# Kernel optimization log

Measured on AMD Instinct MI355X. Metric: run time of the kernel, lower is better.

The kernel has to match this reference:

```python
import jax, jax.numpy as jnp
import numpy as np

N_NODES = 150000
N_EDGES = 4800000
IN_DIM, HID_DIM, OUT_DIM = 1433, 16, 7


def setup_inputs() -> dict:
    key = jax.random.key(0)
    ks = jax.random.split(key, 8)
    features = jax.random.normal(ks[0], (N_NODES, IN_DIM), dtype=jnp.float32)
    edge_src = jax.random.randint(ks[1], (N_EDGES,), 0, N_NODES, dtype=jnp.int32)
    edge_dst = jax.random.randint(ks[2], (N_EDGES,), 0, N_NODES, dtype=jnp.int32)
    adj_vals = jax.random.uniform(ks[3], (N_EDGES,), dtype=jnp.float32)
    W1 = jax.random.normal(ks[4], (IN_DIM, HID_DIM), dtype=jnp.float32) * (1.0 / np.sqrt(IN_DIM))
    b1 = jnp.zeros((HID_DIM,), dtype=jnp.float32)
    W2 = jax.random.normal(ks[5], (HID_DIM, OUT_DIM), dtype=jnp.float32) * (1.0 / np.sqrt(HID_DIM))
    b2 = jnp.zeros((OUT_DIM,), dtype=jnp.float32)
    return {"features": features, "edge_src": edge_src, "edge_dst": edge_dst,
            "adj_vals": adj_vals, "W1": W1, "b1": b1, "W2": W2, "b2": b2}


def _gcn_layer(x, edge_src, edge_dst, adj_vals, W, b):
    # h = A_hat @ (x @ W) + b ; dense transform first since in_dim >= out_dim
    xw = x @ W                                   # [N, d_out]
    msg = adj_vals[:, None] * xw[edge_src]       # [E, d_out] gather
    agg = jax.ops.segment_sum(msg, edge_dst, num_segments=x.shape[0])  # scatter-add
    return agg + b


def reference(features, edge_src, edge_dst, adj_vals, W1, b1, W2, b2):
    h1 = jax.nn.relu(_gcn_layer(features, edge_src, edge_dst, adj_vals, W1, b1))
    # dropout in original forward is a no-op (result discarded) -> omitted
    h2 = _gcn_layer(h1, edge_src, edge_dst, adj_vals, W2, b2)
    return jax.nn.log_softmax(h2, axis=1)
```

## Files before the change

### kernel.cpp

```cpp
#include <hip/hip_runtime.h>
#include <float.h>
#include <stdint.h>

#define IN_DIM 1433
#define HID 16
#define OUTD 7

#define KC 32
#define GROWS 128
#define NT ((IN_DIM + KC - 1) / KC)
#define KLAST (IN_DIM - (NT - 1) * KC)

__global__ __launch_bounds__(256, 4) void gemm1_kernel(
    const float* __restrict__ feat, const float* __restrict__ W1,
    float* __restrict__ xw1, int N)
{
    __shared__ float xs[2][GROWS * KC];
    const int t = threadIdx.x;
    const int lane = t & 63;
    const int wid = t >> 6;
    const int row0 = blockIdx.x * GROWS;
    const long maxElem = (long)N * IN_DIM - 1;

    const int r  = t & (GROWS - 1);
    const int jh = t >> 7;
    const int rx = r & 31;

    float acc[8];
#pragma unroll
    for (int j = 0; j < 8; ++j) acc[j] = 0.f;

    const int jhu = __builtin_amdgcn_readfirstlane(jh);
    const float* __restrict__ wptr = W1 + jhu * 8;

    const int l5 = lane >> 5;
    const int c  = lane & 31;

    auto stage = [&](int buf, int k0) {
#pragma unroll
        for (int i = 0; i < 16; ++i) {
            const int rr = wid * 32 + i * 2 + l5;
            long elem = (long)(row0 + rr) * IN_DIM + k0 + (c ^ (rr & 31));
            if (elem > maxElem) elem = maxElem;
            const float* gp = feat + elem;
            float* lp = &xs[buf][(wid * 32 + i * 2) * KC];
            __builtin_amdgcn_global_load_lds(
                (const __attribute__((address_space(1))) void*)gp,
                (__attribute__((address_space(3))) void*)lp, 4, 0, 0);
        }
    };

#define COMPUTE(buf, k0v, KMAX)                                          \
    {                                                                    \
        const float* xrow = &xs[buf][r * KC];                            \
        const float* wk = wptr + (size_t)(k0v) * HID;                    \
        _Pragma("unroll")                                                \
        for (int kk = 0; kk < (KMAX); ++kk) {                            \
            const float x = xrow[kk ^ rx];                               \
            const float4 wa = *(const float4*)(wk + kk * HID);           \
            const float4 wb = *(const float4*)(wk + kk * HID + 4);       \
            acc[0] += x * wa.x; acc[1] += x * wa.y;                      \
            acc[2] += x * wa.z; acc[3] += x * wa.w;                      \
            acc[4] += x * wb.x; acc[5] += x * wb.y;                      \
            acc[6] += x * wb.z; acc[7] += x * wb.w;                      \
        }                                                                \
    }

    stage(0, 0);
    __syncthreads();
    for (int it = 0; it < NT - 1; ++it) {
        const int cur = it & 1;
        stage(cur ^ 1, (it + 1) * KC);
        COMPUTE(cur, it * KC, KC);
        __syncthreads();
    }
    COMPUTE((NT - 1) & 1, (NT - 1) * KC, KLAST);
#undef COMPUTE

    const int grow = row0 + r;
    if (grow < N) {
        float4* o = (float4*)(xw1 + (size_t)grow * HID + jh * 8);
        o[0] = make_float4(acc[0], acc[1], acc[2], acc[3]);
        o[1] = make_float4(acc[4], acc[5], acc[6], acc[7]);
    }
}

__global__ __launch_bounds__(256) void hist_kernel(
    const int* __restrict__ dst, int* __restrict__ cnt, int E)
{
    const int e = blockIdx.x * 256 + threadIdx.x;
    if (e < E) atomicAdd(&cnt[dst[e]], 1);
}

__global__ __launch_bounds__(256) void scan1_kernel(
    const int* __restrict__ cnt, int* __restrict__ offs,
    int* __restrict__ bsum, int N)
{
    __shared__ int lds[256];
    const int t = threadIdx.x, b = blockIdx.x;
    const int base = b * 1024 + t * 4;
    int c0 = 0, c1 = 0, c2 = 0, c3 = 0;
    if (base + 0 < N) c0 = cnt[base + 0];
    if (base + 1 < N) c1 = cnt[base + 1];
    if (base + 2 < N) c2 = cnt[base + 2];
    if (base + 3 < N) c3 = cnt[base + 3];
    const int s = c0 + c1 + c2 + c3;
    lds[t] = s;
    __syncthreads();
    for (int off = 1; off < 256; off <<= 1) {
        int v = (t >= off) ? lds[t - off] : 0;
        __syncthreads();
        lds[t] += v;
        __syncthreads();
    }
    const int excl = lds[t] - s;
    if (t == 255) bsum[b] = lds[255];
    int run = excl;
    if (base + 0 < N) { offs[base + 0] = run; run += c0; }
    if (base + 1 < N) { offs[base + 1] = run; run += c1; }
    if (base + 2 < N) { offs[base + 2] = run; run += c2; }
    if (base + 3 < N) { offs[base + 3] = run; run += c3; }
}

__global__ __launch_bounds__(256) void scan2_kernel(
    const int* __restrict__ bsum, int* __restrict__ bbase, int NB)
{
    __shared__ int lds[256];
    const int t = threadIdx.x;
    const int v = (t < NB) ? bsum[t] : 0;
    lds[t] = v;
    __syncthreads();
    for (int off = 1; off < 256; off <<= 1) {
        int u = (t >= off) ? lds[t - off] : 0;
        __syncthreads();
        lds[t] += u;
        __syncthreads();
    }
    bbase[t] = lds[t] - v;
}

__global__ __launch_bounds__(256) void scan3_kernel(
    int* __restrict__ offs, int* __restrict__ cursor,
    const int* __restrict__ bbase, int N, int E)
{
    const int t = threadIdx.x, b = blockIdx.x;
    const int add = bbase[b];
    const int base = b * 1024 + t * 4;
#pragma unroll
    for (int i = 0; i < 4; ++i) {
        const int idx = base + i;
        if (idx < N) {
            const int v = offs[idx] + add;
            offs[idx] = v;
            cursor[idx] = v;
        }
    }
    if (b == 0 && t == 0) offs[N] = E;
}

__global__ __launch_bounds__(256) void fill_kernel(
    const int* __restrict__ src, const int* __restrict__ dst,
    const float* __restrict__ a, int* __restrict__ cursor,
    uint2* __restrict__ pairs, int E)
{
    const int e = blockIdx.x * 256 + threadIdx.x;
    if (e >= E) return;
    const int d = dst[e];
    const int pos = atomicAdd(&cursor[d], 1);
    pairs[pos] = make_uint2((unsigned)src[e], __float_as_uint(a[e]));
}

__global__ __launch_bounds__(256) void gather1_kernel(
    const uint2* __restrict__ pairs, const int* __restrict__ offs,
    const float* __restrict__ xw1, const float* __restrict__ b1,
    const float* __restrict__ W2, float* __restrict__ xw2, int N)
{
    __shared__ float w2s[HID * OUTD];
    const int t = threadIdx.x;
    if (t < HID * OUTD) w2s[t] = W2[t];
    __syncthreads();
    const int lane = t & 63;
    const int r = blockIdx.x * 4 + (t >> 6);
    if (r >= N) return;
    const int dim = lane & 15;
    const int grp = lane >> 4;
    const int start = offs[r], end = offs[r + 1];
    float acc0 = 0.f, acc1 = 0.f;
    int e = start + grp;
    for (; e + 4 < end; e += 8) {
        const uint2 p0 = pairs[e];
        const uint2 p1 = pairs[e + 4];
        acc0 += __uint_as_float(p0.y) * xw1[(long)p0.x * HID + dim];
        acc1 += __uint_as_float(p1.y) * xw1[(long)p1.x * HID + dim];
    }
    if (e < end) {
        const uint2 p0 = pairs[e];
        acc0 += __uint_as_float(p0.y) * xw1[(long)p0.x * HID + dim];
    }
    float acc = acc0 + acc1;
    acc += __shfl_xor(acc, 16);
    acc += __shfl_xor(acc, 32);
    const float h = fmaxf(acc + b1[dim], 0.f);
    float sacc = 0.f;
    const int c = (dim < OUTD) ? dim : 0;
#pragma unroll
    for (int j = 0; j < HID; ++j) {
        const float hj = __shfl(h, j);
        sacc += hj * w2s[j * OUTD + c];
    }
    if (lane < 8) xw2[(long)r * 8 + lane] = (lane < OUTD) ? sacc : 0.f;
}

__global__ __launch_bounds__(256) void gather2_kernel(
    const uint2* __restrict__ pairs, const int* __restrict__ offs,
    const float* __restrict__ xw2, const float* __restrict__ b2,
    float* __restrict__ out, int N)
{
    const int t = threadIdx.x;
    const int lane = t & 63;
    const int r = blockIdx.x * 4 + (t >> 6);
    if (r >= N) return;
    const int dim = lane & 7;
    const int grp = lane >> 3;
    const int start = offs[r], end = offs[r + 1];
    float acc0 = 0.f, acc1 = 0.f;
    int e = start + grp;
    for (; e + 8 < end; e += 16) {
        const uint2 p0 = pairs[e];
        const uint2 p1 = pairs[e + 8];
        acc0 += __uint_as_float(p0.y) * xw2[(long)p0.x * 8 + dim];
        acc1 += __uint_as_float(p1.y) * xw2[(long)p1.x * 8 + dim];
    }
    if (e < end) {
        const uint2 p0 = pairs[e];
        acc0 += __uint_as_float(p0.y) * xw2[(long)p0.x * 8 + dim];
    }
    float acc = acc0 + acc1;
    acc += __shfl_xor(acc, 8);
    acc += __shfl_xor(acc, 16);
    acc += __shfl_xor(acc, 32);
    float x = (dim < OUTD) ? (acc + b2[dim]) : -FLT_MAX;
    float m = x;
    m = fmaxf(m, __shfl_xor(m, 1));
    m = fmaxf(m, __shfl_xor(m, 2));
    m = fmaxf(m, __shfl_xor(m, 4));
    const float ev = (dim < OUTD) ? expf(x - m) : 0.f;
    float ssum = ev;
    ssum += __shfl_xor(ssum, 1);
    ssum += __shfl_xor(ssum, 2);
    ssum += __shfl_xor(ssum, 4);
    const float lg = logf(ssum);
    if (lane < OUTD) out[(long)r * OUTD + lane] = x - m - lg;
}

extern "C" void kernel_launch(void* const* d_in, const int* in_sizes, int n_in,
                              void* d_out, int out_size, void* d_ws, size_t ws_size,
                              hipStream_t stream)
{
    const float* feat  = (const float*)d_in[0];
    const int*   esrc  = (const int*)d_in[1];
    const int*   edst  = (const int*)d_in[2];
    const float* avals = (const float*)d_in[3];
    const float* W1    = (const float*)d_in[4];
    const float* b1    = (const float*)d_in[5];
    const float* W2    = (const float*)d_in[6];
    const float* b2    = (const float*)d_in[7];
    float* out = (float*)d_out;

    const int N = in_sizes[0] / IN_DIM;
    const int E = in_sizes[1];
    const int NB = (N + 1023) / 1024;

    char* p = (char*)d_ws;
    float* xw1   = (float*)p; p += (size_t)N * HID * sizeof(float);
    float* xw2   = (float*)p; p += (size_t)N * 8 * sizeof(float);
    int*   cnt   = (int*)p;   p += (size_t)N * sizeof(int);
    int*   offs  = (int*)p;   p += (size_t)(N + 1) * sizeof(int);
    int*   cursor= (int*)p;   p += (size_t)N * sizeof(int);
    int*   bsum  = (int*)p;   p += 256 * sizeof(int);
    int*   bbase = (int*)p;   p += 256 * sizeof(int);
    p = (char*)(((uintptr_t)p + 15) & ~(uintptr_t)15);
    uint2* pairs = (uint2*)p;

    hipMemsetAsync(cnt, 0, (size_t)N * sizeof(int), stream);

    gemm1_kernel<<<(N + GROWS - 1) / GROWS, 256, 0, stream>>>(feat, W1, xw1, N);

    hist_kernel<<<(E + 255) / 256, 256, 0, stream>>>(edst, cnt, E);
    scan1_kernel<<<NB, 256, 0, stream>>>(cnt, offs, bsum, N);
    scan2_kernel<<<1, 256, 0, stream>>>(bsum, bbase, NB);
    scan3_kernel<<<NB, 256, 0, stream>>>(offs, cursor, bbase, N, E);
    fill_kernel<<<(E + 255) / 256, 256, 0, stream>>>(esrc, edst, avals, cursor, pairs, E);

    gather1_kernel<<<(N + 3) / 4, 256, 0, stream>>>(pairs, offs, xw1, b1, W2, xw2, N);
    gather2_kernel<<<(N + 3) / 4, 256, 0, stream>>>(pairs, offs, xw2, b2, out, N);
}
```

Baseline: 1.055 ms.

## Fuse degree histogram into GEMM1 and retile to 64-row blocks with K=128 chunks

```diff
diff --git a/kernel.cpp b/kernel.cpp
--- a/kernel.cpp
+++ b/kernel.cpp
@@ -6,90 +6,78 @@
 #define HID 16
 #define OUTD 7
 
-#define KC 32
-#define GROWS 128
-#define NT ((IN_DIM + KC - 1) / KC)
-#define KLAST (IN_DIM - (NT - 1) * KC)
-
-__global__ __launch_bounds__(256, 4) void gemm1_kernel(
+#define BR 64
+#define KC2 128
+#define NT2 ((IN_DIM + KC2 - 1) / KC2)
+#define KLAST2 (IN_DIM - (NT2 - 1) * KC2)
+
+__global__ __launch_bounds__(256, 2) void gemm1_hist_kernel(
     const float* __restrict__ feat, const float* __restrict__ W1,
-    float* __restrict__ xw1, int N)
-{
-    __shared__ float xs[2][GROWS * KC];
+    float* __restrict__ xw1, int N,
+    const int* __restrict__ edst, int* __restrict__ cnt, int E, int EPB)
+{
+    __shared__ float xs[2][BR * KC2];
     const int t = threadIdx.x;
     const int lane = t & 63;
-    const int wid = t >> 6;
-    const int row0 = blockIdx.x * GROWS;
+    const int w = t >> 6;
+    const int row0 = blockIdx.x * BR;
     const long maxElem = (long)N * IN_DIM - 1;
 
-    const int r  = t & (GROWS - 1);
-    const int jh = t >> 7;
+    const int r  = t & 63;
     const int rx = r & 31;
-
-    float acc[8];
-#pragma unroll
-    for (int j = 0; j < 8; ++j) acc[j] = 0.f;
-
-    const int jhu = __builtin_amdgcn_readfirstlane(jh);
-    const float* __restrict__ wptr = W1 + jhu * 8;
-
-    const int l5 = lane >> 5;
-    const int c  = lane & 31;
+    const int wq = __builtin_amdgcn_readfirstlane(w);
+
+    float acc[4] = {0.f, 0.f, 0.f, 0.f};
 
     auto stage = [&](int buf, int k0) {
 #pragma unroll
-        for (int i = 0; i < 16; ++i) {
-            const int rr = wid * 32 + i * 2 + l5;
-            long elem = (long)(row0 + rr) * IN_DIM + k0 + (c ^ (rr & 31));
+        for (int i = 0; i < 32; ++i) {
+            const int ri = w * 16 + (i >> 1);
+            const int h  = i & 1;
+            const int slot = h * 64 + lane;
+            const int c = (slot & ~31) | ((slot & 31) ^ (ri & 31));
+            long elem = (long)(row0 + ri) * IN_DIM + k0 + c;
             if (elem > maxElem) elem = maxElem;
             const float* gp = feat + elem;
-            float* lp = &xs[buf][(wid * 32 + i * 2) * KC];
+            float* lp = &xs[buf][ri * KC2 + h * 64];
             __builtin_amdgcn_global_load_lds(
                 (const __attribute__((address_space(1))) void*)gp,
                 (__attribute__((address_space(3))) void*)lp, 4, 0, 0);
         }
     };
 
-#define COMPUTE(buf, k0v, KMAX)                                          \
-    {                                                                    \
-        const float* xrow = &xs[buf][r * KC];                            \
-        const float* wk = wptr + (size_t)(k0v) * HID;                    \
-        _Pragma("unroll")                                                \
-        for (int kk = 0; kk < (KMAX); ++kk) {                            \
-            const float x = xrow[kk ^ rx];                               \
-            const float4 wa = *(const float4*)(wk + kk * HID);           \
-            const float4 wb = *(const float4*)(wk + kk * HID + 4);       \
-            acc[0] += x * wa.x; acc[1] += x * wa.y;                      \
-            acc[2] += x * wa.z; acc[3] += x * wa.w;                      \
-            acc[4] += x * wb.x; acc[5] += x * wb.y;                      \
-            acc[6] += x * wb.z; acc[7] += x * wb.w;                      \
-        }                                                                \
+#define COMPUTE2(buf, k0v, KMAX)                                            \
+    {                                                                       \
+        const float* xrow = &xs[buf][r * KC2];                              \
+        _Pragma("unroll 8")                                                 \
+        for (int kk = 0; kk < (KMAX); ++kk) {                               \
+            const float x = xrow[(kk & ~31) | ((kk & 31) ^ rx)];            \
+            const float4 wv = *(const float4*)(W1 +                         \
+                (size_t)((k0v) + kk) * HID + wq * 4);                       \
+            acc[0] += x * wv.x; acc[1] += x * wv.y;                         \
+            acc[2] += x * wv.z; acc[3] += x * wv.w;                         \
+        }                                                                   \
     }
 
     stage(0, 0);
     __syncthreads();
-    for (int it = 0; it < NT - 1; ++it) {
-        const int cur = it & 1;
-        stage(cur ^ 1, (it + 1) * KC);
-        COMPUTE(cur, it * KC, KC);
-        __syncthreads();
-    }
-    COMPUTE((NT - 1) & 1, (NT - 1) * KC, KLAST);
-#undef COMPUTE
+    for (int it = 0; it < NT2 - 1; ++it) {
+        stage((it & 1) ^ 1, (it + 1) * KC2);
+        COMPUTE2(it & 1, it * KC2, KC2);
+        __syncthreads();
+    }
+    COMPUTE2((NT2 - 1) & 1, (NT2 - 1) * KC2, KLAST2);
+#undef COMPUTE2
 
     const int grow = row0 + r;
-    if (grow < N) {
-        float4* o = (float4*)(xw1 + (size_t)grow * HID + jh * 8);
-        o[0] = make_float4(acc[0], acc[1], acc[2], acc[3]);
-        o[1] = make_float4(acc[4], acc[5], acc[6], acc[7]);
-    }
-}
-
-__global__ __launch_bounds__(256) void hist_kernel(
-    const int* __restrict__ dst, int* __restrict__ cnt, int E)
-{
-    const int e = blockIdx.x * 256 + threadIdx.x;
-    if (e < E) atomicAdd(&cnt[dst[e]], 1);
+    if (grow < N)
+        *(float4*)(xw1 + (size_t)grow * HID + wq * 4) =
+            make_float4(acc[0], acc[1], acc[2], acc[3]);
+
+    const int e0 = blockIdx.x * EPB;
+    const int e1 = min(e0 + EPB, E);
+    for (int e = e0 + t; e < e1; e += 256)
+        atomicAdd(&cnt[edst[e]], 1);
 }
 
 __global__ __launch_bounds__(256) void scan1_kernel(
@@ -284,9 +272,10 @@
 
     hipMemsetAsync(cnt, 0, (size_t)N * sizeof(int), stream);
 
-    gemm1_kernel<<<(N + GROWS - 1) / GROWS, 256, 0, stream>>>(feat, W1, xw1, N);
-
-    hist_kernel<<<(E + 255) / 256, 256, 0, stream>>>(edst, cnt, E);
+    const int G = (N + BR - 1) / BR;
+    const int EPB = (E + G - 1) / G;
+    gemm1_hist_kernel<<<G, 256, 0, stream>>>(feat, W1, xw1, N, edst, cnt, E, EPB);
+
     scan1_kernel<<<NB, 256, 0, stream>>>(cnt, offs, bsum, N);
     scan2_kernel<<<1, 256, 0, stream>>>(bsum, bbase, NB);
     scan3_kernel<<<NB, 256, 0, stream>>>(offs, cursor, bbase, N, E);
```

After: 1.440 ms. 36.5% more time.

## Deepen GEMM1 pipeline to 4 stages and stage W1 in LDS

Applied to the files above, without the earlier changes.

```diff
diff --git a/kernel.cpp b/kernel.cpp
--- a/kernel.cpp
+++ b/kernel.cpp
@@ -6,83 +6,97 @@
 #define HID 16
 #define OUTD 7
 
-#define KC 32
-#define GROWS 128
-#define NT ((IN_DIM + KC - 1) / KC)
-#define KLAST (IN_DIM - (NT - 1) * KC)
-
-__global__ __launch_bounds__(256, 4) void gemm1_kernel(
+#define BRW 128
+#define KCW 32
+#define DEPTH 4
+#define NTW ((IN_DIM + KCW - 1) / KCW)
+#define KLASTW (IN_DIM - (NTW - 1) * KCW)
+#define WN (IN_DIM * HID)
+
+#define AS1 __attribute__((address_space(1)))
+#define AS3 __attribute__((address_space(3)))
+
+__global__ __launch_bounds__(512, 1) void gemm1_kernel(
     const float* __restrict__ feat, const float* __restrict__ W1,
     float* __restrict__ xw1, int N)
 {
-    __shared__ float xs[2][GROWS * KC];
+    __shared__ float xs[DEPTH][BRW * KCW];
+    __shared__ float wl[WN];
     const int t = threadIdx.x;
     const int lane = t & 63;
-    const int wid = t >> 6;
-    const int row0 = blockIdx.x * GROWS;
+    const int w = t >> 6;
+    const int row0 = blockIdx.x * BRW;
     const long maxElem = (long)N * IN_DIM - 1;
 
-    const int r  = t & (GROWS - 1);
-    const int jh = t >> 7;
+    for (int i0 = 0; i0 < WN; i0 += 512) {
+        if (i0 + t < WN) {
+            __builtin_amdgcn_global_load_lds(
+                (const AS1 void*)(W1 + i0 + t),
+                (AS3 void*)(wl + i0 + w * 64), 4, 0, 0);
+        }
+    }
+    __syncthreads();
+
+    const int r  = t & (BRW - 1);
     const int rx = r & 31;
-
-    float acc[8];
-#pragma unroll
-    for (int j = 0; j < 8; ++j) acc[j] = 0.f;
-
-    const int jhu = __builtin_amdgcn_readfirstlane(jh);
-    const float* __restrict__ wptr = W1 + jhu * 8;
+    const int q  = t >> 7;
+    float acc[4] = {0.f, 0.f, 0.f, 0.f};
 
     const int l5 = lane >> 5;
     const int c  = lane & 31;
 
     auto stage = [&](int buf, int k0) {
 #pragma unroll
-        for (int i = 0; i < 16; ++i) {
-            const int rr = wid * 32 + i * 2 + l5;
+        for (int i = 0; i < 8; ++i) {
+            const int rr = w * 16 + i * 2 + l5;
             long elem = (long)(row0 + rr) * IN_DIM + k0 + (c ^ (rr & 31));
             if (elem > maxElem) elem = maxElem;
-            const float* gp = feat + elem;
-            float* lp = &xs[buf][(wid * 32 + i * 2) * KC];
             __builtin_amdgcn_global_load_lds(
-                (const __attribute__((address_space(1))) void*)gp,
-                (__attribute__((address_space(3))) void*)lp, 4, 0, 0);
+                (const AS1 void*)(feat + elem),
+                (AS3 void*)(&xs[buf][(w * 16 + i * 2) * KCW]), 4, 0, 0);
         }
     };
 
 #define COMPUTE(buf, k0v, KMAX)                                          \
     {                                                                    \
-        const float* xrow = &xs[buf][r * KC];                            \
-        const float* wk = wptr + (size_t)(k0v) * HID;                    \
+        const float* xrow = &xs[buf][r * KCW];                           \
+        const float* wb = wl + (size_t)(k0v) * HID + q * 4;              \
         _Pragma("unroll")                                                \
         for (int kk = 0; kk < (KMAX); ++kk) {                            \
             const float x = xrow[kk ^ rx];                               \
-            const float4 wa = *(const float4*)(wk + kk * HID);           \
-            const float4 wb = *(const float4*)(wk + kk * HID + 4);       \
-            acc[0] += x * wa.x; acc[1] += x * wa.y;                      \
-            acc[2] += x * wa.z; acc[3] += x * wa.w;                      \
-            acc[4] += x * wb.x; acc[5] += x * wb.y;                      \
-            acc[6] += x * wb.z; acc[7] += x * wb.w;                      \
+            const float4 wv = *(const float4*)(wb + kk * HID);           \
+            acc[0] += x * wv.x; acc[1] += x * wv.y;                      \
+            acc[2] += x * wv.z; acc[3] += x * wv.w;                      \
         }                                                                \
     }
 
+#define WAITBAR(Nimm)                                                    \
+    asm volatile("s_waitcnt vmcnt(" #Nimm ")" ::: "memory");             \
+    __builtin_amdgcn_sched_barrier(0);                                   \
+    __builtin_amdgcn_s_barrier();                                        \
+    __builtin_amdgcn_sched_barrier(0);
+
     stage(0, 0);
-    __syncthreads();
-    for (int it = 0; it < NT - 1; ++it) {
-        const int cur = it & 1;
-        stage(cur ^ 1, (it + 1) * KC);
-        COMPUTE(cur, it * KC, KC);
-        __syncthreads();
-    }
-    COMPUTE((NT - 1) & 1, (NT - 1) * KC, KLAST);
+    stage(1, KCW);
+    stage(2, 2 * KCW);
+    for (int it = 0; it < NTW - 3; ++it) {
+        WAITBAR(16);
+        stage((it + 3) & (DEPTH - 1), (it + 3) * KCW);
+        COMPUTE(it & (DEPTH - 1), it * KCW, KCW);
+    }
+    WAITBAR(16);
+    COMPUTE((NTW - 3) & (DEPTH - 1), (NTW - 3) * KCW, KCW);
+    WAITBAR(8);
+    COMPUTE((NTW - 2) & (DEPTH - 1), (NTW - 2) * KCW, KCW);
+    WAITBAR(0);
+    COMPUTE((NTW - 1) & (DEPTH - 1), (NTW - 1) * KCW, KLASTW);
 #undef COMPUTE
+#undef WAITBAR
 
     const int grow = row0 + r;
-    if (grow < N) {
-        float4* o = (float4*)(xw1 + (size_t)grow * HID + jh * 8);
-        o[0] = make_float4(acc[0], acc[1], acc[2], acc[3]);
-        o[1] = make_float4(acc[4], acc[5], acc[6], acc[7]);
-    }
+    if (grow < N)
+        *(float4*)(xw1 + (size_t)grow * HID + q * 4) =
+            make_float4(acc[0], acc[1], acc[2], acc[3]);
 }
 
 __global__ __launch_bounds__(256) void hist_kernel(
@@ -284,7 +298,7 @@
 
     hipMemsetAsync(cnt, 0, (size_t)N * sizeof(int), stream);
 
-    gemm1_kernel<<<(N + GROWS - 1) / GROWS, 256, 0, stream>>>(feat, W1, xw1, N);
+    gemm1_kernel<<<(N + BRW - 1) / BRW, 512, 0, stream>>>(feat, W1, xw1, N);
 
     hist_kernel<<<(E + 255) / 256, 256, 0, stream>>>(edst, cnt, E);
     scan1_kernel<<<NB, 256, 0, stream>>>(cnt, offs, bsum, N);
```

New measurement: 1.240 ms. 1.18x slower.

## Retile GEMM1 for vector LDS reads and vectorize gather kernels with float4 loads

Applied to the files above, without the earlier changes.

```diff
diff --git a/kernel.cpp b/kernel.cpp
--- a/kernel.cpp
+++ b/kernel.cpp
@@ -7,82 +7,88 @@
 #define OUTD 7
 
 #define KC 32
-#define GROWS 128
+#define GROWS 64
 #define NT ((IN_DIM + KC - 1) / KC)
 #define KLAST (IN_DIM - (NT - 1) * KC)
 
-__global__ __launch_bounds__(256, 4) void gemm1_kernel(
+#define AS1 __attribute__((address_space(1)))
+#define AS3 __attribute__((address_space(3)))
+
+__global__ __launch_bounds__(256, 8) void gemm1_kernel(
     const float* __restrict__ feat, const float* __restrict__ W1,
     float* __restrict__ xw1, int N)
 {
     __shared__ float xs[2][GROWS * KC];
     const int t = threadIdx.x;
     const int lane = t & 63;
-    const int wid = t >> 6;
+    const int w = t >> 6;
     const int row0 = blockIdx.x * GROWS;
     const long maxElem = (long)N * IN_DIM - 1;
 
-    const int r  = t & (GROWS - 1);
-    const int jh = t >> 7;
-    const int rx = r & 31;
-
-    float acc[8];
-#pragma unroll
-    for (int j = 0; j < 8; ++j) acc[j] = 0.f;
-
-    const int jhu = __builtin_amdgcn_readfirstlane(jh);
-    const float* __restrict__ wptr = W1 + jhu * 8;
-
-    const int l5 = lane >> 5;
-    const int c  = lane & 31;
+    const int r  = t & 63;
+    const int rb = r & 7;
+    const int q4 = __builtin_amdgcn_readfirstlane(w) * 4;
+
+    float acc[4] = {0.f, 0.f, 0.f, 0.f};
 
     auto stage = [&](int buf, int k0) {
 #pragma unroll
-        for (int i = 0; i < 16; ++i) {
-            const int rr = wid * 32 + i * 2 + l5;
-            long elem = (long)(row0 + rr) * IN_DIM + k0 + (c ^ (rr & 31));
+        for (int i = 0; i < 8; ++i) {
+            const int ri = (i * 4 + w) * 2 + (lane >> 5);
+            const int cs = lane & 31;
+            const int gcol = (cs & 3) | (((cs >> 2) ^ (ri & 7)) << 2);
+            long elem = (long)(row0 + ri) * IN_DIM + k0 + gcol;
             if (elem > maxElem) elem = maxElem;
-            const float* gp = feat + elem;
-            float* lp = &xs[buf][(wid * 32 + i * 2) * KC];
             __builtin_amdgcn_global_load_lds(
-                (const __attribute__((address_space(1))) void*)gp,
-                (__attribute__((address_space(3))) void*)lp, 4, 0, 0);
+                (const AS1 void*)(feat + elem),
+                (AS3 void*)(&xs[buf][(i * 4 + w) * 64]), 4, 0, 0);
         }
     };
 
-#define COMPUTE(buf, k0v, KMAX)                                          \
-    {                                                                    \
-        const float* xrow = &xs[buf][r * KC];                            \
-        const float* wk = wptr + (size_t)(k0v) * HID;                    \
-        _Pragma("unroll")                                                \
-        for (int kk = 0; kk < (KMAX); ++kk) {                            \
-            const float x = xrow[kk ^ rx];                               \
-            const float4 wa = *(const float4*)(wk + kk * HID);           \
-            const float4 wb = *(const float4*)(wk + kk * HID + 4);       \
-            acc[0] += x * wa.x; acc[1] += x * wa.y;                      \
-            acc[2] += x * wa.z; acc[3] += x * wa.w;                      \
-            acc[4] += x * wb.x; acc[5] += x * wb.y;                      \
-            acc[6] += x * wb.z; acc[7] += x * wb.w;                      \
-        }                                                                \
+#define COMPUTE(buf, k0v, KMAX)                                              \
+    {                                                                        \
+        const float* xrow = &xs[buf][r * KC];                                \
+        _Pragma("unroll")                                                    \
+        for (int b = 0; b < ((KMAX) >> 2); ++b) {                            \
+            const float4 xv = *(const float4*)&xrow[((b ^ rb) << 2)];        \
+            const float* wk = W1 + (size_t)((k0v) + 4 * b) * HID + q4;       \
+            const float4 w0 = *(const float4*)(wk);                          \
+            const float4 w1 = *(const float4*)(wk + HID);                    \
+            const float4 w2 = *(const float4*)(wk + 2 * HID);                \
+            const float4 w3 = *(const float4*)(wk + 3 * HID);                \
+            acc[0] += xv.x * w0.x; acc[1] += xv.x * w0.y;                    \
+            acc[2] += xv.x * w0.z; acc[3] += xv.x * w0.w;                    \
+            acc[0] += xv.y * w1.x; acc[1] += xv.y * w1.y;                    \
+            acc[2] += xv.y * w1.z; acc[3] += xv.y * w1.w;                    \
+            acc[0] += xv.z * w2.x; acc[1] += xv.z * w2.y;                    \
+            acc[2] += xv.z * w2.z; acc[3] += xv.z * w2.w;                    \
+            acc[0] += xv.w * w3.x; acc[1] += xv.w * w3.y;                    \
+            acc[2] += xv.w * w3.z; acc[3] += xv.w * w3.w;                    \
+        }                                                                    \
+        if ((KMAX) & 3) {                     \
+            const int b = (KMAX) >> 2;                                       \
+            const float4 xv = *(const float4*)&xrow[((b ^ rb) << 2)];        \
+            const float* wk = W1 + (size_t)((k0v) + 4 * b) * HID + q4;       \
+            const float4 w0 = *(const float4*)(wk);                          \
+            acc[0] += xv.x * w0.x; acc[1] += xv.x * w0.y;                    \
+            acc[2] += xv.x * w0.z; acc[3] += xv.x * w0.w;                    \
+        }                                                                    \
     }
 
     stage(0, 0);
     __syncthreads();
     for (int it = 0; it < NT - 1; ++it) {
-        const int cur = it & 1;
-        stage(cur ^ 1, (it + 1) * KC);
-        COMPUTE(cur, it * KC, KC);
+        stage((it & 1) ^ 1, (it + 1) * KC);
+        COMPUTE(it & 1, it * KC, KC);
         __syncthreads();
     }
     COMPUTE((NT - 1) & 1, (NT - 1) * KC, KLAST);
 #undef COMPUTE
 
     const int grow = row0 + r;
-    if (grow < N) {
-        float4* o = (float4*)(xw1 + (size_t)grow * HID + jh * 8);
-        o[0] = make_float4(acc[0], acc[1], acc[2], acc[3]);
-        o[1] = make_float4(acc[4], acc[5], acc[6], acc[7]);
-    }
+    if (grow < N)
+        *(float4*)(xw1 + (size_t)grow * HID + q4) =
+            make_float4(acc[0], acc[1], acc[2], acc[3]);
 }
 
 __global__ __launch_bounds__(256) void hist_kernel(
@@ -182,33 +188,56 @@
     const int lane = t & 63;
     const int r = blockIdx.x * 4 + (t >> 6);
     if (r >= N) return;
-    const int dim = lane & 15;
-    const int grp = lane >> 4;
+    const int g = lane >> 2;
+    const int c = lane & 3;
     const int start = offs[r], end = offs[r + 1];
-    float acc0 = 0.f, acc1 = 0.f;
-    int e = start + grp;
-    for (; e + 4 < end; e += 8) {
+    float4 acc = make_float4(0.f, 0.f, 0.f, 0.f);
+    int e = start + g;
+    for (; e + 16 < end; e += 32) {
         const uint2 p0 = pairs[e];
-        const uint2 p1 = pairs[e + 4];
-        acc0 += __uint_as_float(p0.y) * xw1[(long)p0.x * HID + dim];
-        acc1 += __uint_as_float(p1.y) * xw1[(long)p1.x * HID + dim];
+        const uint2 p1 = pairs[e + 16];
+        const float4 v0 = *(const float4*)(xw1 + (size_t)p0.x * HID + c * 4);
+        const float4 v1 = *(const float4*)(xw1 + (size_t)p1.x * HID + c * 4);
+        const float a0 = __uint_as_float(p0.y);
+        const float a1 = __uint_as_float(p1.y);
+        acc.x += a0 * v0.x + a1 * v1.x;
+        acc.y += a0 * v0.y + a1 * v1.y;
+        acc.z += a0 * v0.z + a1 * v1.z;
+        acc.w += a0 * v0.w + a1 * v1.w;
     }
     if (e < end) {
         const uint2 p0 = pairs[e];
-        acc0 += __uint_as_float(p0.y) * xw1[(long)p0.x * HID + dim];
-    }
-    float acc = acc0 + acc1;
-    acc += __shfl_xor(acc, 16);
-    acc += __shfl_xor(acc, 32);
-    const float h = fmaxf(acc + b1[dim], 0.f);
+        const float4 v0 = *(const float4*)(xw1 + (size_t)p0.x * HID + c * 4);
+        const float a0 = __uint_as_float(p0.y);
+        acc.x += a0 * v0.x; acc.y += a0 * v0.y;
+        acc.z += a0 * v0.z; acc.w += a0 * v0.w;
+    }
+#pragma unroll
+    for (int m = 4; m < 64; m <<= 1) {
+        acc.x += __shfl_xor(acc.x, m);
+        acc.y += __shfl_xor(acc.y, m);
+        acc.z += __shfl_xor(acc.z, m);
+        acc.w += __shfl_xor(acc.w, m);
+    }
+    const float4 b1v = ((const float4*)b1)[c];
+    float4 h;
+    h.x = fmaxf(acc.x + b1v.x, 0.f);
+    h.y = fmaxf(acc.y + b1v.y, 0.f);
+    h.z = fmaxf(acc.z + b1v.z, 0.f);
+    h.w = fmaxf(acc.w + b1v.w, 0.f);
+    float hh[16];
+#pragma unroll
+    for (int cc = 0; cc < 4; ++cc) {
+        hh[cc * 4 + 0] = __shfl(h.x, cc);
+        hh[cc * 4 + 1] = __shfl(h.y, cc);
+        hh[cc * 4 + 2] = __shfl(h.z, cc);
+        hh[cc * 4 + 3] = __shfl(h.w, cc);
+    }
+    const int col = (lane & 7) < OUTD ? (lane & 7) : 0;
     float sacc = 0.f;
-    const int c = (dim < OUTD) ? dim : 0;
-#pragma unroll
-    for (int j = 0; j < HID; ++j) {
-        const float hj = __shfl(h, j);
-        sacc += hj * w2s[j * OUTD + c];
-    }
-    if (lane < 8) xw2[(long)r * 8 + lane] = (lane < OUTD) ? sacc : 0.f;
+#pragma unroll
+    for (int j = 0; j < HID; ++j) sacc += hh[j] * w2s[j * OUTD + col];
+    if (lane < 8) xw2[(size_t)r * 8 + lane] = (lane < OUTD) ? sacc : 0.f;
 }
 
 __global__ __launch_bounds__(256) void gather2_kernel(
@@ -220,37 +249,48 @@
     const int lane = t & 63;
     const int r = blockIdx.x * 4 + (t >> 6);
     if (r >= N) return;
-    const int dim = lane & 7;
-    const int grp = lane >> 3;
+    const int g = lane >> 1;
+    const int c = lane & 1;
     const int start = offs[r], end = offs[r + 1];
-    float acc0 = 0.f, acc1 = 0.f;
-    int e = start + grp;
-    for (; e + 8 < end; e += 16) {
-        const uint2 p0 = pairs[e];
-        const uint2 p1 = pairs[e + 8];
-        acc0 += __uint_as_float(p0.y) * xw2[(long)p0.x * 8 + dim];
-        acc1 += __uint_as_float(p1.y) * xw2[(long)p1.x * 8 + dim];
-    }
-    if (e < end) {
-        const uint2 p0 = pairs[e];
-        acc0 += __uint_as_float(p0.y) * xw2[(long)p0.x * 8 + dim];
-    }
-    float acc = acc0 + acc1;
-    acc += __shfl_xor(acc, 8);
-    acc += __shfl_xor(acc, 16);
-    acc += __shfl_xor(acc, 32);
-    float x = (dim < OUTD) ? (acc + b2[dim]) : -FLT_MAX;
-    float m = x;
-    m = fmaxf(m, __shfl_xor(m, 1));
-    m = fmaxf(m, __shfl_xor(m, 2));
-    m = fmaxf(m, __shfl_xor(m, 4));
-    const float ev = (dim < OUTD) ? expf(x - m) : 0.f;
-    float ssum = ev;
-    ssum += __shfl_xor(ssum, 1);
-    ssum += __shfl_xor(ssum, 2);
-    ssum += __shfl_xor(ssum, 4);
-    const float lg = logf(ssum);
-    if (lane < OUTD) out[(long)r * OUTD + lane] = x - m - lg;
+    float4 acc = make_float4(0.f, 0.f, 0.f, 0.f);
+    for (int e = start + g; e < end; e += 32) {
+        const uint2 p = pairs[e];
+        const float4 v = *(const float4*)(xw2 + (size_t)p.x * 8 + c * 4);
+        const float a = __uint_as_float(p.y);
+        acc.x += a * v.x; acc.y += a * v.y;
+        acc.z += a * v.z; acc.w += a * v.w;
+    }
+#pragma unroll
+    for (int m = 2; m < 64; m <<= 1) {
+        acc.x += __shfl_xor(acc.x, m);
+        acc.y += __shfl_xor(acc.y, m);
+        acc.z += __shfl_xor(acc.z, m);
+        acc.w += __shfl_xor(acc.w, m);
+    }
+    float4 x;
+    if (c == 0) {
+        const float4 b2v = *(const float4*)b2;
+        x.x = acc.x + b2v.x; x.y = acc.y + b2v.y;
+        x.z = acc.z + b2v.z; x.w = acc.w + b2v.w;
+    } else {
+        x.x = acc.x + b2[4]; x.y = acc.y + b2[5];
+        x.z = acc.z + b2[6]; x.w = -FLT_MAX;
+    }
+    float mymax = fmaxf(fmaxf(x.x, x.y), x.z);
+    if (c == 0) mymax = fmaxf(mymax, x.w);
+    const float m = fmaxf(mymax, __shfl_xor(mymax, 1));
+    float es = expf(x.x - m) + expf(x.y - m) + expf(x.z - m);
+    if (c == 0) es += expf(x.w - m);
+    const float s = es + __shfl_xor(es, 1);
+    const float lg = logf(s);
+    float* op = out + (size_t)r * OUTD;
+    if (c == 0) {
+        op[0] = x.x - m - lg; op[1] = x.y - m - lg;
+        op[2] = x.z - m - lg; op[3] = x.w - m - lg;
+    } else {
+        op[4] = x.x - m - lg; op[5] = x.y - m - lg;
+        op[6] = x.z - m - lg;
+    }
 }
 
 extern "C" void kernel_launch(void* const* d_in, const int* in_sizes, int n_in,
```

Result: faster. 1.003 ms (-4.9%).
